# Performance work log

Hardware: AMD Instinct MI355X
Metric: run time of the kernel (lower is better)

The kernel has to match this reference:

```python
import jax, jax.numpy as jnp
import numpy as np
from math import sqrt

B, S, E, H = 4, 2048, 1024, 16
DH = E // H  # 64


def setup_inputs() -> dict:
    key = jax.random.key(0)
    ks = jax.random.split(key, 10)
    sc = 0.02
    return {
        "x": jax.random.normal(ks[0], (B, S, E), dtype=jnp.float32),
        # per-head projection weights stacked: [H, E, DH], biases [H, DH]
        "Wq": jax.random.normal(ks[1], (H, E, DH), dtype=jnp.float32) * sc,
        "bq": jax.random.normal(ks[2], (H, DH), dtype=jnp.float32) * sc,
        "Wk": jax.random.normal(ks[3], (H, E, DH), dtype=jnp.float32) * sc,
        "bk": jax.random.normal(ks[4], (H, DH), dtype=jnp.float32) * sc,
        "Wv": jax.random.normal(ks[5], (H, E, DH), dtype=jnp.float32) * sc,
        "bv": jax.random.normal(ks[6], (H, DH), dtype=jnp.float32) * sc,
        "Wo": jax.random.normal(ks[7], (E, E), dtype=jnp.float32) * sc,
        "bo": jax.random.normal(ks[8], (E,), dtype=jnp.float32) * sc,
    }


def reference(x, Wq, bq, Wk, bk, Wv, bv, Wo, bo):
    # Batched QKV projections (equivalent to the per-head Linear loop)
    q = jnp.einsum("bse,hed->bhsd", x, Wq) + bq[None, :, None, :]
    k = jnp.einsum("bse,hed->bhsd", x, Wk) + bk[None, :, None, :]
    v = jnp.einsum("bse,hed->bhsd", x, Wv) + bv[None, :, None, :]
    scores = jnp.einsum("bhsd,bhtd->bhst", q, k) / sqrt(DH)
    # masked=False in the module, so plain softmax over keys
    weights = jax.nn.softmax(scores, axis=-1)
    attn = jnp.einsum("bhst,bhtd->bhsd", weights, v)
    # concat heads: [B,S,H*DH] with head i contiguous (matches torch.cat dim=-1)
    concat = attn.transpose(0, 2, 1, 3).reshape(B, S, H * DH)
    out = concat @ Wo.T if Wo.shape == (E, E) and False else jnp.einsum("bsf,ef->bse", concat, Wo) + bo
    return out
```

## Files before the change

### kernel.cpp

```cpp
#include <hip/hip_runtime.h>
#include <math.h>

#define Bc 4
#define Sc 2048
#define Ec 1024
#define Hc 16
#define DHc 64

typedef unsigned short u16;
typedef __attribute__((ext_vector_type(8))) short short8;
typedef __attribute__((ext_vector_type(4))) float f32x4;
typedef __attribute__((ext_vector_type(2))) unsigned short u16x2;

__device__ __forceinline__ u16 f2bf(float f) {
    unsigned int u = __float_as_uint(f);
    u += 0x7FFFu + ((u >> 16) & 1u);
    return (u16)(u >> 16);
}

__device__ __forceinline__ void gl_lds16(const void* g, void* l) {
    __builtin_amdgcn_global_load_lds(
        (const __attribute__((address_space(1))) unsigned int*)g,
        (__attribute__((address_space(3))) unsigned int*)l,
        16, 0, 0);
}

__global__ __launch_bounds__(256)
void cast_bf16_kernel(const float* __restrict__ in, u16* __restrict__ out, int n8)
{
    int i = blockIdx.x * 256 + threadIdx.x;
    if (i >= n8) return;
    const float* p = in + (size_t)i * 8;
    float4 a = *(const float4*)p;
    float4 b = *(const float4*)(p + 4);
    short8 v;
    v[0] = (short)f2bf(a.x); v[1] = (short)f2bf(a.y);
    v[2] = (short)f2bf(a.z); v[3] = (short)f2bf(a.w);
    v[4] = (short)f2bf(b.x); v[5] = (short)f2bf(b.y);
    v[6] = (short)f2bf(b.z); v[7] = (short)f2bf(b.w);
    *(short8*)(out + (size_t)i * 8) = v;
}

__global__ __launch_bounds__(256)
void transW_kernel(const float* __restrict__ Wq, const float* __restrict__ Wk,
                   const float* __restrict__ Wv, u16* __restrict__ Wtb)
{
    __shared__ float T[64][65];
    const int t = threadIdx.x;
    const int e0 = blockIdx.x * 64;
    const int h = blockIdx.y;
    const int proj = blockIdx.z;
    const float* W = (proj == 0) ? Wq : (proj == 1) ? Wk : Wv;

    #pragma unroll
    for (int i = 0; i < 4; ++i) {
        int fid = t + i * 256;
        int row = fid >> 4, c4 = fid & 15;
        float4 v = *(const float4*)(W + ((size_t)h * Ec + e0 + row) * DHc + c4 * 4);
        T[row][c4 * 4 + 0] = v.x; T[row][c4 * 4 + 1] = v.y;
        T[row][c4 * 4 + 2] = v.z; T[row][c4 * 4 + 3] = v.w;
    }
    __syncthreads();
    const int d = t >> 2, ech = (t & 3) * 16;
    u16* dst = Wtb + ((size_t)(proj * Hc + h) * DHc + d) * Ec + e0 + ech;
    #pragma unroll
    for (int j = 0; j < 16; j += 2) {
        u16x2 v2;
        v2.x = f2bf(T[ech + j][d]);
        v2.y = f2bf(T[ech + j + 1][d]);
        *(u16x2*)(dst + j) = v2;
    }
}

__global__ __launch_bounds__(256)
void qkv_mfma_kernel(const u16* __restrict__ xb, const u16* __restrict__ Wtb,
                     const float* __restrict__ bq, const float* __restrict__ bk,
                     const float* __restrict__ bv,
                     u16* __restrict__ qb, u16* __restrict__ kb, u16* __restrict__ vb)
{
    __shared__ __align__(16) u16 As[128 * 64];
    __shared__ __align__(16) u16 Bs[128 * 64];

    const int t = threadIdx.x;
    const int w = t >> 6, l = t & 63;
    const int wr = w >> 1, wc = w & 1;
    const int mBase = blockIdx.y * 128;
    const int nBase = blockIdx.x * 128;
    const int proj = nBase >> 10;
    const int nIn = nBase & (Ec - 1);
    const int lr = l >> 3, ls = l & 7;
    const int lq = l >> 4, ln = l & 15;

    f32x4 acc[4][4];
    #pragma unroll
    for (int i = 0; i < 4; ++i)
        #pragma unroll
        for (int j = 0; j < 4; ++j) acc[i][j] = (f32x4)0.f;

    for (int k0 = 0; k0 < Ec; k0 += 64) {
        __syncthreads();
        #pragma unroll
        for (int c = 0; c < 8; ++c) {
            int cg = w * 8 + c;
            if (cg < 16) {
                int row = cg * 8 + lr;
                int g = ls ^ (row & 7);
                gl_lds16(xb + ((size_t)(mBase + row)) * Ec + k0 + g * 8,
                         (void*)(As + cg * 512));
            } else {
                int col = (cg - 16) * 8 + lr;
                int g = ls ^ (col & 7);
                gl_lds16(Wtb + ((size_t)proj * Ec + nIn + col) * Ec + k0 + g * 8,
                         (void*)(Bs + (cg - 16) * 512));
            }
        }
        __syncthreads();

        #pragma unroll
        for (int ks = 0; ks < 2; ++ks) {
            short8 af[4], bfr[4];
            int gg = ks * 4 + lq;
            #pragma unroll
            for (int fm = 0; fm < 4; ++fm) {
                int row = wr * 64 + fm * 16 + ln;
                af[fm] = *(const short8*)(As + row * 64 + ((gg ^ (row & 7)) * 8));
            }
            #pragma unroll
            for (int fn = 0; fn < 4; ++fn) {
                int col = wc * 64 + fn * 16 + ln;
                bfr[fn] = *(const short8*)(Bs + col * 64 + ((gg ^ (col & 7)) * 8));
            }
            #pragma unroll
            for (int fm = 0; fm < 4; ++fm)
                #pragma unroll
                for (int fn = 0; fn < 4; ++fn)
                    acc[fm][fn] = __builtin_amdgcn_mfma_f32_16x16x32_bf16(
                        af[fm], bfr[fn], acc[fm][fn], 0, 0, 0);
        }
    }

    const float* bias = (proj == 0) ? bq : (proj == 1) ? bk : bv;
    #pragma unroll
    for (int fn = 0; fn < 4; ++fn) {
        int n = nBase + wc * 64 + fn * 16 + ln;
        int cc = n & (Ec - 1);
        int hh = cc >> 6, d = cc & 63;
        float bv_ = bias[cc];
        #pragma unroll
        for (int fm = 0; fm < 4; ++fm) {
            #pragma unroll
            for (int r = 0; r < 4; ++r) {
                int m = mBase + wr * 64 + fm * 16 + lq * 4 + r;
                int b = m >> 11, s = m & (Sc - 1);
                int bh = b * Hc + hh;
                float vv = acc[fm][fn][r] + bv_;
                if (proj == 0)      qb[((size_t)bh * Sc + s) * DHc + d] = f2bf(vv * 0.18033688011f);
                else if (proj == 1) kb[((size_t)bh * Sc + s) * DHc + d] = f2bf(vv);
                else                vb[((size_t)bh * DHc + d) * Sc + s] = f2bf(vv);
            }
        }
    }
}

__global__ __launch_bounds__(512, 4)
void attn_mfma_kernel(const u16* __restrict__ qb, const u16* __restrict__ kb,
                      const u16* __restrict__ vb, u16* __restrict__ concatb)
{
    __shared__ __align__(16) u16 Kt[2][64 * 64];
    __shared__ __align__(16) u16 Vt[2][64 * 64];
    __shared__ __align__(16) u16 Ps[8 * 32 * 64];

    const int t = threadIdx.x;
    const int w = t >> 6, l = t & 63;
    const int qt = blockIdx.x, h = blockIdx.y, b = blockIdx.z;
    const int bh = b * Hc + h;
    const int lq = l >> 4, ln = l & 15;
    const int lr = l >> 3, ls = l & 7;
    const int sw = ln & 7;

    const u16* qp = qb + ((size_t)bh * Sc + qt * 256 + w * 32) * DHc;
    const u16* kp = kb + (size_t)bh * Sc * DHc;
    const u16* vp = vb + (size_t)bh * DHc * Sc;
    u16* pw = Ps + w * (32 * 64);

    const int cg = w * 2;

    short8 qf[2][2];
    #pragma unroll
    for (int qg = 0; qg < 2; ++qg)
        #pragma unroll
        for (int ks = 0; ks < 2; ++ks)
            qf[qg][ks] = *(const short8*)(qp + (qg * 16 + ln) * DHc + ks * 32 + lq * 8);

    f32x4 o[2][4];
    #pragma unroll
    for (int qg = 0; qg < 2; ++qg)
        #pragma unroll
        for (int fd = 0; fd < 4; ++fd) o[qg][fd] = (f32x4)0.f;
    float m_i[2] = {-1e30f, -1e30f}, l_i[2] = {0.f, 0.f};

    #pragma unroll
    for (int c = 0; c < 2; ++c) {
        int g2 = cg + c;
        if (g2 < 8) {
            int row = g2 * 8 + lr;
            int g = ls ^ (row & 7);
            gl_lds16(kp + ((size_t)row) * DHc + g * 8, (void*)(Kt[0] + g2 * 512));
        } else {
            int d = (g2 - 8) * 8 + lr;
            int g = ls ^ (d & 7);
            gl_lds16(vp + (size_t)d * Sc + g * 8, (void*)(Vt[0] + (g2 - 8) * 512));
        }
    }
    asm volatile("s_waitcnt vmcnt(0)" ::: "memory");
    __syncthreads();

    for (int kt = 0; kt < Sc / 64; ++kt) {
        const int cur = kt & 1;
        if (kt + 1 < Sc / 64) {
            const int nxt = cur ^ 1;
            #pragma unroll
            for (int c = 0; c < 2; ++c) {
                int g2 = cg + c;
                if (g2 < 8) {
                    int row = g2 * 8 + lr;
                    int g = ls ^ (row & 7);
                    gl_lds16(kp + ((size_t)((kt + 1) * 64 + row)) * DHc + g * 8,
                             (void*)(Kt[nxt] + g2 * 512));
                } else {
                    int d = (g2 - 8) * 8 + lr;
                    int g = ls ^ (d & 7);
                    gl_lds16(vp + (size_t)d * Sc + (kt + 1) * 64 + g * 8,
                             (void*)(Vt[nxt] + (g2 - 8) * 512));
                }
            }
        }

        f32x4 s[2][4];
        #pragma unroll
        for (int qg = 0; qg < 2; ++qg)
            #pragma unroll
            for (int fn = 0; fn < 4; ++fn) s[qg][fn] = (f32x4)0.f;
        __builtin_amdgcn_s_setprio(1);
        #pragma unroll
        for (int ks = 0; ks < 2; ++ks) {
            int gg = ks * 4 + lq;
            #pragma unroll
            for (int fn = 0; fn < 4; ++fn) {
                int key = fn * 16 + ln;
                short8 kf = *(const short8*)(Kt[cur] + key * 64 + ((gg ^ sw) * 8));
                s[0][fn] = __builtin_amdgcn_mfma_f32_16x16x32_bf16(kf, qf[0][ks], s[0][fn], 0, 0, 0);
                s[1][fn] = __builtin_amdgcn_mfma_f32_16x16x32_bf16(kf, qf[1][ks], s[1][fn], 0, 0, 0);
            }
        }
        __builtin_amdgcn_s_setprio(0);

        float pmax[2];
        #pragma unroll
        for (int qg = 0; qg < 2; ++qg) {
            float m0 = fmaxf(fmaxf(s[qg][0][0], s[qg][0][1]), fmaxf(s[qg][0][2], s[qg][0][3]));
            float m1 = fmaxf(fmaxf(s[qg][1][0], s[qg][1][1]), fmaxf(s[qg][1][2], s[qg][1][3]));
            float m2 = fmaxf(fmaxf(s[qg][2][0], s[qg][2][1]), fmaxf(s[qg][2][2], s[qg][2][3]));
            float m3 = fmaxf(fmaxf(s[qg][3][0], s[qg][3][1]), fmaxf(s[qg][3][2], s[qg][3][3]));
            float mx = fmaxf(fmaxf(m0, m1), fmaxf(m2, m3));
            mx = fmaxf(mx, __shfl_xor(mx, 16));
            mx = fmaxf(mx, __shfl_xor(mx, 32));
            pmax[qg] = mx;
        }
        bool need = (pmax[0] > m_i[0] + 8.f) || (pmax[1] > m_i[1] + 8.f);
        if (__any(need)) {
            #pragma unroll
            for (int qg = 0; qg < 2; ++qg) {
                float nm = fmaxf(m_i[qg], pmax[qg]);
                float ef = exp2f(m_i[qg] - nm);
                l_i[qg] *= ef;
                m_i[qg] = nm;
                #pragma unroll
                for (int r = 0; r < 4; ++r) {
                    float efr = __shfl(ef, lq * 4 + r);
                    #pragma unroll
                    for (int fd = 0; fd < 4; ++fd) o[qg][fd][r] *= efr;
                }
            }
        }
        #pragma unroll
        for (int qg = 0; qg < 2; ++qg) {
            float p[4][4];
            float sum = 0.f;
            #pragma unroll
            for (int fn = 0; fn < 4; ++fn)
                #pragma unroll
                for (int r = 0; r < 4; ++r) {
                    p[fn][r] = exp2f(s[qg][fn][r] - m_i[qg]);
                    sum += p[fn][r];
                }
            sum += __shfl_xor(sum, 16);
            sum += __shfl_xor(sum, 32);
            l_i[qg] += sum;
            #pragma unroll
            for (int fn = 0; fn < 4; ++fn) {
                unsigned int pa, pb;
                asm("v_cvt_pk_bf16_f32 %0, %1, %2" : "=v"(pa) : "v"(p[fn][0]), "v"(p[fn][1]));
                asm("v_cvt_pk_bf16_f32 %0, %1, %2" : "=v"(pb) : "v"(p[fn][2]), "v"(p[fn][3]));
                uint2 u; u.x = pa; u.y = pb;
                *(uint2*)(pw + (qg * 16 + ln) * 64 +
                          (((2 * fn + (lq >> 1)) ^ sw) << 3) + (lq & 1) * 4) = u;
            }
        }
        asm volatile("s_waitcnt lgkmcnt(0)" ::: "memory");

        __builtin_amdgcn_s_setprio(1);
        #pragma unroll
        for (int c = 0; c < 2; ++c) {
            int gg = c * 4 + lq;
            short8 pf0 = *(const short8*)(pw + ln * 64 + ((gg ^ sw) << 3));
            short8 pf1 = *(const short8*)(pw + (16 + ln) * 64 + ((gg ^ sw) << 3));
            #pragma unroll
            for (int fd = 0; fd < 4; ++fd) {
                int d = fd * 16 + ln;
                short8 vf = *(const short8*)(Vt[cur] + d * 64 + ((gg ^ sw) << 3));
                o[0][fd] = __builtin_amdgcn_mfma_f32_16x16x32_bf16(pf0, vf, o[0][fd], 0, 0, 0);
                o[1][fd] = __builtin_amdgcn_mfma_f32_16x16x32_bf16(pf1, vf, o[1][fd], 0, 0, 0);
            }
        }
        __builtin_amdgcn_s_setprio(0);

        asm volatile("s_waitcnt vmcnt(0)" ::: "memory");
        __syncthreads();
    }

    #pragma unroll
    for (int qg = 0; qg < 2; ++qg) {
        #pragma unroll
        for (int r = 0; r < 4; ++r) {
            float lr_ = __shfl(l_i[qg], lq * 4 + r);
            float inv = 1.f / lr_;
            int q = qt * 256 + w * 32 + qg * 16 + lq * 4 + r;
            #pragma unroll
            for (int fd = 0; fd < 4; ++fd) {
                int d = h * DHc + fd * 16 + ln;
                concatb[((size_t)b * Sc + q) * Ec + d] = f2bf(o[qg][fd][r] * inv);
            }
        }
    }
}

__global__ __launch_bounds__(256)
void oproj_mfma_kernel(const u16* __restrict__ cb, const u16* __restrict__ Wob,
                       const float* __restrict__ bo, float* __restrict__ out)
{
    __shared__ __align__(16) u16 As[128 * 64];
    __shared__ __align__(16) u16 Bs[128 * 64];

    const int t = threadIdx.x;
    const int w = t >> 6, l = t & 63;
    const int wr = w >> 1, wc = w & 1;
    const int mBase = blockIdx.y * 128;
    const int nBase = blockIdx.x * 128;
    const int lr = l >> 3, ls = l & 7;
    const int lq = l >> 4, ln = l & 15;

    f32x4 acc[4][4];
    #pragma unroll
    for (int i = 0; i < 4; ++i)
        #pragma unroll
        for (int j = 0; j < 4; ++j) acc[i][j] = (f32x4)0.f;

    for (int k0 = 0; k0 < Ec; k0 += 64) {
        __syncthreads();
        #pragma unroll
        for (int c = 0; c < 8; ++c) {
            int cg = w * 8 + c;
            if (cg < 16) {
                int row = cg * 8 + lr;
                int g = ls ^ (row & 7);
                gl_lds16(cb + ((size_t)(mBase + row)) * Ec + k0 + g * 8,
                         (void*)(As + cg * 512));
            } else {
                int col = (cg - 16) * 8 + lr;
                int g = ls ^ (col & 7);
                gl_lds16(Wob + ((size_t)(nBase + col)) * Ec + k0 + g * 8,
                         (void*)(Bs + (cg - 16) * 512));
            }
        }
        __syncthreads();

        #pragma unroll
        for (int ks = 0; ks < 2; ++ks) {
            short8 af[4], bfr[4];
            int gg = ks * 4 + lq;
            #pragma unroll
            for (int fm = 0; fm < 4; ++fm) {
                int row = wr * 64 + fm * 16 + ln;
                af[fm] = *(const short8*)(As + row * 64 + ((gg ^ (row & 7)) * 8));
            }
            #pragma unroll
            for (int fn = 0; fn < 4; ++fn) {
                int col = wc * 64 + fn * 16 + ln;
                bfr[fn] = *(const short8*)(Bs + col * 64 + ((gg ^ (col & 7)) * 8));
            }
            #pragma unroll
            for (int fm = 0; fm < 4; ++fm)
                #pragma unroll
                for (int fn = 0; fn < 4; ++fn)
                    acc[fm][fn] = __builtin_amdgcn_mfma_f32_16x16x32_bf16(
                        af[fm], bfr[fn], acc[fm][fn], 0, 0, 0);
        }
    }

    #pragma unroll
    for (int fn = 0; fn < 4; ++fn) {
        int n = nBase + wc * 64 + fn * 16 + ln;
        float bb = bo[n];
        #pragma unroll
        for (int fm = 0; fm < 4; ++fm) {
            #pragma unroll
            for (int r = 0; r < 4; ++r) {
                int m = mBase + wr * 64 + fm * 16 + lq * 4 + r;
                out[(size_t)m * Ec + n] = acc[fm][fn][r] + bb;
            }
        }
    }
}

extern "C" void kernel_launch(void* const* d_in, const int* in_sizes, int n_in,
                              void* d_out, int out_size, void* d_ws, size_t ws_size,
                              hipStream_t stream)
{
    const float* x  = (const float*)d_in[0];
    const float* Wq = (const float*)d_in[1];
    const float* bq = (const float*)d_in[2];
    const float* Wk = (const float*)d_in[3];
    const float* bk = (const float*)d_in[4];
    const float* Wv = (const float*)d_in[5];
    const float* bv = (const float*)d_in[6];
    const float* Wo = (const float*)d_in[7];
    const float* bo = (const float*)d_in[8];
    float* out = (float*)d_out;

    char* ws = (char*)d_ws;
    u16* xb   = (u16*)(ws);
    u16* Wtb  = (u16*)(ws + (16u << 20));
    u16* Wob  = (u16*)(ws + (22u << 20));
    u16* qbuf = (u16*)(ws + (24u << 20));
    u16* kbuf = (u16*)(ws + (40u << 20));
    u16* vbuf = (u16*)(ws + (56u << 20));
    u16* cbuf = (u16*)(ws + (72u << 20));

    cast_bf16_kernel<<<(Bc * Sc * Ec / 8 + 255) / 256, 256, 0, stream>>>(x, xb, Bc * Sc * Ec / 8);
    cast_bf16_kernel<<<(Ec * Ec / 8 + 255) / 256, 256, 0, stream>>>(Wo, Wob, Ec * Ec / 8);
    dim3 gt(Ec / 64, Hc, 3);
    transW_kernel<<<gt, 256, 0, stream>>>(Wq, Wk, Wv, Wtb);

    dim3 g1(3 * Ec / 128, (Bc * Sc) / 128);
    qkv_mfma_kernel<<<g1, 256, 0, stream>>>(xb, Wtb, bq, bk, bv, qbuf, kbuf, vbuf);

    dim3 g2(Sc / 256, Hc, Bc);
    attn_mfma_kernel<<<g2, 512, 0, stream>>>(qbuf, kbuf, vbuf, cbuf);

    dim3 g3(Ec / 128, (Bc * Sc) / 128);
    oproj_mfma_kernel<<<g3, 256, 0, stream>>>(cbuf, Wob, bo, out);
}
```

Baseline: 262.8 us.

## Switch attention to 32x32x16 MFMA and keep P in registers

Rewrites the attention inner loop to use 32x32x16 bf16 MFMA tiles, computing S transposed so that each lane owns one query column. The softmax probabilities are converted to bf16 and exchanged between half-waves with cross-lane shuffles instead of being written to and read back from the per-wave LDS buffer. This removes the P round-trip through shared memory and the lgkmcnt wait, and reduces the per-row max/sum shuffles. In exchange it adds shuffle/select overhead and uses larger accumulator register sets, which may affect occupancy.

```diff
diff --git a/kernel.cpp b/kernel.cpp
--- a/kernel.cpp
+++ b/kernel.cpp
@@ -10,7 +10,10 @@
 typedef unsigned short u16;
 typedef __attribute__((ext_vector_type(8))) short short8;
 typedef __attribute__((ext_vector_type(4))) float f32x4;
+typedef __attribute__((ext_vector_type(16))) float f32x16;
 typedef __attribute__((ext_vector_type(2))) unsigned short u16x2;
+
+union pk8 { unsigned int u[4]; short8 v; };
 
 __device__ __forceinline__ u16 f2bf(float f) {
     unsigned int u = __float_as_uint(f);
@@ -168,36 +171,28 @@
 {
     __shared__ __align__(16) u16 Kt[2][64 * 64];
     __shared__ __align__(16) u16 Vt[2][64 * 64];
-    __shared__ __align__(16) u16 Ps[8 * 32 * 64];
 
     const int t = threadIdx.x;
     const int w = t >> 6, l = t & 63;
     const int qt = blockIdx.x, h = blockIdx.y, b = blockIdx.z;
     const int bh = b * Hc + h;
-    const int lq = l >> 4, ln = l & 15;
+    const int hi = l >> 5, l5 = l & 31;
     const int lr = l >> 3, ls = l & 7;
-    const int sw = ln & 7;
-
-    const u16* qp = qb + ((size_t)bh * Sc + qt * 256 + w * 32) * DHc;
+    const int sw5 = l5 & 7;
+
+    const u16* qp = qb + ((size_t)bh * Sc + qt * 256 + w * 32 + l5) * DHc;
     const u16* kp = kb + (size_t)bh * Sc * DHc;
     const u16* vp = vb + (size_t)bh * DHc * Sc;
-    u16* pw = Ps + w * (32 * 64);
 
     const int cg = w * 2;
 
-    short8 qf[2][2];
-    #pragma unroll
-    for (int qg = 0; qg < 2; ++qg)
-        #pragma unroll
-        for (int ks = 0; ks < 2; ++ks)
-            qf[qg][ks] = *(const short8*)(qp + (qg * 16 + ln) * DHc + ks * 32 + lq * 8);
-
-    f32x4 o[2][4];
-    #pragma unroll
-    for (int qg = 0; qg < 2; ++qg)
-        #pragma unroll
-        for (int fd = 0; fd < 4; ++fd) o[qg][fd] = (f32x4)0.f;
-    float m_i[2] = {-1e30f, -1e30f}, l_i[2] = {0.f, 0.f};
+    short8 qf[4];
+    #pragma unroll
+    for (int ks = 0; ks < 4; ++ks)
+        qf[ks] = *(const short8*)(qp + ks * 16 + hi * 8);
+
+    f32x16 o0 = (f32x16)0.f, o1 = (f32x16)0.f;
+    float m_i = -1e30f, l_i = 0.f;
 
     #pragma unroll
     for (int c = 0; c < 2; ++c) {
@@ -236,112 +231,95 @@
             }
         }
 
-        f32x4 s[2][4];
-        #pragma unroll
-        for (int qg = 0; qg < 2; ++qg)
-            #pragma unroll
-            for (int fn = 0; fn < 4; ++fn) s[qg][fn] = (f32x4)0.f;
+        f32x16 s0 = (f32x16)0.f, s1 = (f32x16)0.f;
         __builtin_amdgcn_s_setprio(1);
         #pragma unroll
-        for (int ks = 0; ks < 2; ++ks) {
-            int gg = ks * 4 + lq;
-            #pragma unroll
-            for (int fn = 0; fn < 4; ++fn) {
-                int key = fn * 16 + ln;
-                short8 kf = *(const short8*)(Kt[cur] + key * 64 + ((gg ^ sw) * 8));
-                s[0][fn] = __builtin_amdgcn_mfma_f32_16x16x32_bf16(kf, qf[0][ks], s[0][fn], 0, 0, 0);
-                s[1][fn] = __builtin_amdgcn_mfma_f32_16x16x32_bf16(kf, qf[1][ks], s[1][fn], 0, 0, 0);
-            }
+        for (int ks = 0; ks < 4; ++ks) {
+            int slot = ((2 * ks + hi) ^ sw5) * 8;
+            short8 kf0 = *(const short8*)(Kt[cur] + (l5) * 64 + slot);
+            short8 kf1 = *(const short8*)(Kt[cur] + (32 + l5) * 64 + slot);
+            s0 = __builtin_amdgcn_mfma_f32_32x32x16_bf16(kf0, qf[ks], s0, 0, 0, 0);
+            s1 = __builtin_amdgcn_mfma_f32_32x32x16_bf16(kf1, qf[ks], s1, 0, 0, 0);
         }
         __builtin_amdgcn_s_setprio(0);
 
-        float pmax[2];
-        #pragma unroll
-        for (int qg = 0; qg < 2; ++qg) {
-            float m0 = fmaxf(fmaxf(s[qg][0][0], s[qg][0][1]), fmaxf(s[qg][0][2], s[qg][0][3]));
-            float m1 = fmaxf(fmaxf(s[qg][1][0], s[qg][1][1]), fmaxf(s[qg][1][2], s[qg][1][3]));
-            float m2 = fmaxf(fmaxf(s[qg][2][0], s[qg][2][1]), fmaxf(s[qg][2][2], s[qg][2][3]));
-            float m3 = fmaxf(fmaxf(s[qg][3][0], s[qg][3][1]), fmaxf(s[qg][3][2], s[qg][3][3]));
-            float mx = fmaxf(fmaxf(m0, m1), fmaxf(m2, m3));
-            mx = fmaxf(mx, __shfl_xor(mx, 16));
-            mx = fmaxf(mx, __shfl_xor(mx, 32));
-            pmax[qg] = mx;
-        }
-        bool need = (pmax[0] > m_i[0] + 8.f) || (pmax[1] > m_i[1] + 8.f);
+        float pm = fmaxf(s0[0], s0[1]);
+        #pragma unroll
+        for (int r = 2; r < 16; ++r) pm = fmaxf(pm, s0[r]);
+        #pragma unroll
+        for (int r = 0; r < 16; ++r) pm = fmaxf(pm, s1[r]);
+        pm = fmaxf(pm, __shfl_xor(pm, 32));
+
+        bool need = pm > m_i + 8.f;
         if (__any(need)) {
-            #pragma unroll
-            for (int qg = 0; qg < 2; ++qg) {
-                float nm = fmaxf(m_i[qg], pmax[qg]);
-                float ef = exp2f(m_i[qg] - nm);
-                l_i[qg] *= ef;
-                m_i[qg] = nm;
-                #pragma unroll
-                for (int r = 0; r < 4; ++r) {
-                    float efr = __shfl(ef, lq * 4 + r);
-                    #pragma unroll
-                    for (int fd = 0; fd < 4; ++fd) o[qg][fd][r] *= efr;
-                }
-            }
-        }
-        #pragma unroll
-        for (int qg = 0; qg < 2; ++qg) {
-            float p[4][4];
-            float sum = 0.f;
-            #pragma unroll
-            for (int fn = 0; fn < 4; ++fn)
-                #pragma unroll
-                for (int r = 0; r < 4; ++r) {
-                    p[fn][r] = exp2f(s[qg][fn][r] - m_i[qg]);
-                    sum += p[fn][r];
-                }
-            sum += __shfl_xor(sum, 16);
-            sum += __shfl_xor(sum, 32);
-            l_i[qg] += sum;
-            #pragma unroll
-            for (int fn = 0; fn < 4; ++fn) {
-                unsigned int pa, pb;
-                asm("v_cvt_pk_bf16_f32 %0, %1, %2" : "=v"(pa) : "v"(p[fn][0]), "v"(p[fn][1]));
-                asm("v_cvt_pk_bf16_f32 %0, %1, %2" : "=v"(pb) : "v"(p[fn][2]), "v"(p[fn][3]));
-                uint2 u; u.x = pa; u.y = pb;
-                *(uint2*)(pw + (qg * 16 + ln) * 64 +
-                          (((2 * fn + (lq >> 1)) ^ sw) << 3) + (lq & 1) * 4) = u;
-            }
-        }
-        asm volatile("s_waitcnt lgkmcnt(0)" ::: "memory");
+            float nm = fmaxf(m_i, pm);
+            float ef = exp2f(m_i - nm);
+            l_i *= ef;
+            m_i = nm;
+            #pragma unroll
+            for (int r = 0; r < 16; ++r) {
+                int qrow = (r & 3) + 8 * (r >> 2) + 4 * hi;
+                float efq = __shfl(ef, qrow);
+                o0[r] *= efq; o1[r] *= efq;
+            }
+        }
+
+        float sum = 0.f;
+
+#define PROC_KG(SV, KG)                                                         \
+        {                                                                       \
+            float p_[16];                                                       \
+            _Pragma("unroll")                                                   \
+            for (int r = 0; r < 16; ++r) {                                      \
+                p_[r] = exp2f(SV[r] - m_i);                                     \
+                sum += p_[r];                                                   \
+            }                                                                   \
+            unsigned int W_[8];                                                 \
+            _Pragma("unroll")                                                   \
+            for (int i = 0; i < 8; ++i)                                         \
+                asm("v_cvt_pk_bf16_f32 %0, %1, %2"                              \
+                    : "=v"(W_[i]) : "v"(p_[2 * i]), "v"(p_[2 * i + 1]));        \
+            unsigned int r0 = __shfl_xor(hi ? W_[0] : W_[2], 32);               \
+            unsigned int r1 = __shfl_xor(hi ? W_[1] : W_[3], 32);               \
+            unsigned int r2 = __shfl_xor(hi ? W_[4] : W_[6], 32);               \
+            unsigned int r3 = __shfl_xor(hi ? W_[5] : W_[7], 32);               \
+            pk8 a0, a1;                                                         \
+            a0.u[0] = hi ? r0 : W_[0];  a0.u[1] = hi ? r1 : W_[1];              \
+            a0.u[2] = hi ? W_[2] : r0;  a0.u[3] = hi ? W_[3] : r1;              \
+            a1.u[0] = hi ? r2 : W_[4];  a1.u[1] = hi ? r3 : W_[5];              \
+            a1.u[2] = hi ? W_[6] : r2;  a1.u[3] = hi ? W_[7] : r3;              \
+            _Pragma("unroll")                                                   \
+            for (int ksl = 0; ksl < 2; ++ksl) {                                 \
+                int slot = (((KG * 4 + ksl * 2 + hi)) ^ sw5) * 8;               \
+                short8 vf0 = *(const short8*)(Vt[cur] + (l5) * 64 + slot);      \
+                short8 vf1 = *(const short8*)(Vt[cur] + (32 + l5) * 64 + slot); \
+                short8 pa = ksl ? a1.v : a0.v;                                  \
+                o0 = __builtin_amdgcn_mfma_f32_32x32x16_bf16(pa, vf0, o0, 0, 0, 0); \
+                o1 = __builtin_amdgcn_mfma_f32_32x32x16_bf16(pa, vf1, o1, 0, 0, 0); \
+            }                                                                   \
+        }
 
         __builtin_amdgcn_s_setprio(1);
-        #pragma unroll
-        for (int c = 0; c < 2; ++c) {
-            int gg = c * 4 + lq;
-            short8 pf0 = *(const short8*)(pw + ln * 64 + ((gg ^ sw) << 3));
-            short8 pf1 = *(const short8*)(pw + (16 + ln) * 64 + ((gg ^ sw) << 3));
-            #pragma unroll
-            for (int fd = 0; fd < 4; ++fd) {
-                int d = fd * 16 + ln;
-                short8 vf = *(const short8*)(Vt[cur] + d * 64 + ((gg ^ sw) << 3));
-                o[0][fd] = __builtin_amdgcn_mfma_f32_16x16x32_bf16(pf0, vf, o[0][fd], 0, 0, 0);
-                o[1][fd] = __builtin_amdgcn_mfma_f32_16x16x32_bf16(pf1, vf, o[1][fd], 0, 0, 0);
-            }
-        }
+        PROC_KG(s0, 0)
+        PROC_KG(s1, 1)
         __builtin_amdgcn_s_setprio(0);
+#undef PROC_KG
+
+        sum += __shfl_xor(sum, 32);
+        l_i += sum;
 
         asm volatile("s_waitcnt vmcnt(0)" ::: "memory");
         __syncthreads();
     }
 
     #pragma unroll
-    for (int qg = 0; qg < 2; ++qg) {
-        #pragma unroll
-        for (int r = 0; r < 4; ++r) {
-            float lr_ = __shfl(l_i[qg], lq * 4 + r);
-            float inv = 1.f / lr_;
-            int q = qt * 256 + w * 32 + qg * 16 + lq * 4 + r;
-            #pragma unroll
-            for (int fd = 0; fd < 4; ++fd) {
-                int d = h * DHc + fd * 16 + ln;
-                concatb[((size_t)b * Sc + q) * Ec + d] = f2bf(o[qg][fd][r] * inv);
-            }
-        }
+    for (int r = 0; r < 16; ++r) {
+        int qrow = (r & 3) + 8 * (r >> 2) + 4 * hi;
+        float inv = 1.f / __shfl(l_i, qrow);
+        int q = qt * 256 + w * 32 + qrow;
+        u16* dst = concatb + ((size_t)b * Sc + q) * Ec + h * DHc + l5;
+        dst[0]  = f2bf(o0[r] * inv);
+        dst[32] = f2bf(o1[r] * inv);
     }
 }
 
```

Result: faster. 244.4 us (-7.0%).
